# Performance work log

Measured on AMD Instinct MI355X. Metric: run time of the kernel, lower is better.

## Reference

```python
import jax, jax.numpy as jnp
import numpy as np

B, T, HE, H = 32, 2048, 512, 512


def setup_inputs() -> dict:
    key = jax.random.key(0)
    ks = jax.random.split(key, 10)
    s_e = 1.0 / np.sqrt(HE)
    s_h = 1.0 / np.sqrt(H)
    return {
        "x": jax.random.normal(ks[0], (B, T, HE), dtype=jnp.float32),
        "wu_i": jax.random.normal(ks[1], (HE, H), dtype=jnp.float32) * s_e,
        "wu_h": jax.random.normal(ks[2], (H, H), dtype=jnp.float32) * s_h,
        "bu": jax.random.normal(ks[3], (H,), dtype=jnp.float32) * s_h,
        "wr_i": jax.random.normal(ks[4], (HE, H), dtype=jnp.float32) * s_e,
        "wr_h": jax.random.normal(ks[5], (H, H), dtype=jnp.float32) * s_h,
        "br": jax.random.normal(ks[6], (H,), dtype=jnp.float32) * s_h,
        "wc_i": jax.random.normal(ks[7], (HE, H), dtype=jnp.float32) * s_e,
        "wc_h": jax.random.normal(ks[8], (H, H), dtype=jnp.float32) * s_h,
        "bc": jax.random.normal(ks[9], (H,), dtype=jnp.float32) * s_h,
    }


def reference(x, wu_i, wu_h, bu, wr_i, wr_h, br, wc_i, wc_h, bc):
    # Precompute input projections for all timesteps (one big GEMM each).
    u_in_x = jnp.einsum("bte,eh->bth", x, wu_i) + bu  # (B,T,H)
    r_in_x = jnp.einsum("bte,eh->bth", x, wr_i) + br
    c_in_x = jnp.einsum("bte,eh->bth", x, wc_i) + bc

    h0 = jnp.zeros((x.shape[0], wu_h.shape[0]), dtype=x.dtype)

    def step(h_prev, inputs):
        u_x, r_x, c_x = inputs
        u = jax.nn.sigmoid(u_x + h_prev @ wu_h)
        r = jax.nn.sigmoid(r_x + h_prev @ wr_h)
        # Faithful to source: r * (h_prev @ wc_h) (reset applied after matmul)
        c = jnp.tanh(c_x + r * (h_prev @ wc_h))
        h = (1.0 - u) * h_prev + u * c
        return h, h

    # scan over time: move T to leading axis
    xs = (
        jnp.swapaxes(u_in_x, 0, 1),
        jnp.swapaxes(r_in_x, 0, 1),
        jnp.swapaxes(c_in_x, 0, 1),
    )
    _, ys = jax.lax.scan(step, h0, xs)  # ys: (T,B,H)
    return jnp.swapaxes(ys, 0, 1)  # (B,T,H)
```

## Files before the change

### kernel.cpp

```cpp
#include <hip/hip_runtime.h>
#include <hip/hip_bf16.h>
#include <hip/hip_fp16.h>
#include <stdint.h>

#define BB 32
#define TT 2048
#define HH 512
#define MM (BB*TT)

typedef __attribute__((ext_vector_type(8))) short bf16x8;
typedef __attribute__((ext_vector_type(4))) float f32x4;
typedef __attribute__((ext_vector_type(2))) float f32x2;
typedef __attribute__((ext_vector_type(4))) unsigned short us4;
typedef __attribute__((ext_vector_type(8))) unsigned short us8;
typedef unsigned long long u64;

__device__ __forceinline__ unsigned short f2bf(float f) {
  __hip_bfloat16 h = __float2bfloat16(f);
  return *reinterpret_cast<unsigned short*>(&h);
}
__device__ __forceinline__ float bf2f(unsigned short u) {
  return __uint_as_float(((unsigned int)u) << 16);
}

__device__ __forceinline__ void wg_barrier_lgkm() {
  asm volatile("s_waitcnt lgkmcnt(0)\n\ts_barrier" ::: "memory");
}

__device__ __forceinline__ float fast_sigmoid(float x) {
  float e = __expf(-x);
  return __builtin_amdgcn_rcpf(1.f + e);
}
__device__ __forceinline__ float fast_tanh(float x) {
  float xc = fminf(fmaxf(x, -15.f), 15.f);
  float e2 = __expf(2.f * xc);
  return (e2 - 1.f) * __builtin_amdgcn_rcpf(e2 + 1.f);
}

__global__ void wconv_kernel(const float* __restrict__ wu, const float* __restrict__ wr,
                             const float* __restrict__ wc,
                             unsigned short* __restrict__ wuT, unsigned short* __restrict__ wrT,
                             unsigned short* __restrict__ wcTh, unsigned short* __restrict__ wcTl) {
  int idx = blockIdx.x * 256 + threadIdx.x;
  int n = idx >> 9, k = idx & 511;
  int src = k * HH + n;
  wuT[idx] = f2bf(wu[src]);
  wrT[idx] = f2bf(wr[src]);
  float v = wc[src];
  unsigned short hi = f2bf(v);
  wcTh[idx] = hi;
  wcTl[idx] = f2bf(v - bf2f(hi));
}

template<int MODE>
__global__ __launch_bounds__(256) void proj_gemm(
    const float* __restrict__ X,
    const unsigned short* __restrict__ B0T,
    const unsigned short* __restrict__ B1T,
    const float* __restrict__ bias0,
    const float* __restrict__ bias1,
    void* __restrict__ outp) {
  __shared__ __attribute__((aligned(16))) unsigned short Ah[128][72];
  __shared__ __attribute__((aligned(16))) unsigned short Al[128][72];
  __shared__ __attribute__((aligned(16))) unsigned short Bs0[64][72];
  __shared__ __attribute__((aligned(16))) unsigned short Bs1[64][72];
  const int tid = threadIdx.x;
  const int w = tid >> 6, l = tid & 63;
  const int lr = l & 15, lk = l >> 4;
  const int rowBase = blockIdx.x * 128;
  const int colBase = blockIdx.y * 64;

  f32x4 acc0[2][4], acc1[2][4];
  const f32x4 zero = {0.f, 0.f, 0.f, 0.f};
  #pragma unroll
  for (int m = 0; m < 2; ++m)
    #pragma unroll
    for (int n = 0; n < 4; ++n) { acc0[m][n] = zero; acc1[m][n] = zero; }

  for (int kt = 0; kt < 8; ++kt) {
    #pragma unroll
    for (int i = 0; i < 8; ++i) {
      int idx = tid + 256 * i;
      int r = idx >> 4, c4 = idx & 15;
      float4 v = *reinterpret_cast<const float4*>(
          X + (size_t)(rowBase + r) * HH + kt * 64 + c4 * 4);
      us4 hv;
      hv.x = f2bf(v.x); hv.y = f2bf(v.y); hv.z = f2bf(v.z); hv.w = f2bf(v.w);
      *reinterpret_cast<us4*>(&Ah[r][c4 * 4]) = hv;
      if (MODE == 1) {
        us4 lv;
        lv.x = f2bf(v.x - bf2f(hv.x)); lv.y = f2bf(v.y - bf2f(hv.y));
        lv.z = f2bf(v.z - bf2f(hv.z)); lv.w = f2bf(v.w - bf2f(hv.w));
        *reinterpret_cast<us4*>(&Al[r][c4 * 4]) = lv;
      }
    }
    #pragma unroll
    for (int i = 0; i < 2; ++i) {
      int idx = tid + 256 * i;
      int n = idx >> 3, k8 = idx & 7;
      const size_t go = (size_t)(colBase + n) * HH + kt * 64 + k8 * 8;
      *reinterpret_cast<us8*>(&Bs0[n][k8 * 8]) = *reinterpret_cast<const us8*>(B0T + go);
      *reinterpret_cast<us8*>(&Bs1[n][k8 * 8]) = *reinterpret_cast<const us8*>(B1T + go);
    }
    __syncthreads();
    #pragma unroll
    for (int ks = 0; ks < 2; ++ks) {
      const int k0 = ks * 32 + lk * 8;
      bf16x8 a[2], b0[4], b1[4];
      #pragma unroll
      for (int m = 0; m < 2; ++m)
        a[m] = *reinterpret_cast<const bf16x8*>(&Ah[32 * w + 16 * m + lr][k0]);
      #pragma unroll
      for (int n = 0; n < 4; ++n) {
        b0[n] = *reinterpret_cast<const bf16x8*>(&Bs0[16 * n + lr][k0]);
        b1[n] = *reinterpret_cast<const bf16x8*>(&Bs1[16 * n + lr][k0]);
      }
      if (MODE == 1) {
        bf16x8 al[2];
        #pragma unroll
        for (int m = 0; m < 2; ++m)
          al[m] = *reinterpret_cast<const bf16x8*>(&Al[32 * w + 16 * m + lr][k0]);
        #pragma unroll
        for (int m = 0; m < 2; ++m)
          #pragma unroll
          for (int n = 0; n < 4; ++n) {
            acc0[m][n] = __builtin_amdgcn_mfma_f32_16x16x32_bf16(a[m],  b0[n], acc0[m][n], 0, 0, 0);
            acc0[m][n] = __builtin_amdgcn_mfma_f32_16x16x32_bf16(a[m],  b1[n], acc0[m][n], 0, 0, 0);
            acc0[m][n] = __builtin_amdgcn_mfma_f32_16x16x32_bf16(al[m], b0[n], acc0[m][n], 0, 0, 0);
          }
      } else {
        #pragma unroll
        for (int m = 0; m < 2; ++m)
          #pragma unroll
          for (int n = 0; n < 4; ++n) {
            acc0[m][n] = __builtin_amdgcn_mfma_f32_16x16x32_bf16(a[m], b0[n], acc0[m][n], 0, 0, 0);
            acc1[m][n] = __builtin_amdgcn_mfma_f32_16x16x32_bf16(a[m], b1[n], acc1[m][n], 0, 0, 0);
          }
      }
    }
    __syncthreads();
  }
  #pragma unroll
  for (int m = 0; m < 2; ++m) {
    #pragma unroll
    for (int n = 0; n < 4; ++n) {
      const int col = colBase + 16 * n + lr;
      const float bv0 = bias0[col];
      const float bv1 = (MODE == 0) ? bias1[col] : 0.f;
      #pragma unroll
      for (int q = 0; q < 4; ++q) {
        const int row = rowBase + 32 * w + 16 * m + lk * 4 + q;
        const size_t o = (size_t)row * HH + col;
        if (MODE == 0) {
          float v0 = acc0[m][n][q] + bv0;
          float v1 = acc1[m][n][q] + bv1;
          unsigned int pk = (unsigned int)__half_as_ushort(__float2half(v0)) |
                            ((unsigned int)__half_as_ushort(__float2half(v1)) << 16);
          reinterpret_cast<unsigned int*>(outp)[o] = pk;
        } else {
          reinterpret_cast<__half*>(outp)[o] = __float2half(acc0[m][n][q] + bv0);
        }
      }
    }
  }
}

__global__ __launch_bounds__(512, 2) void scan_kernel(
    const float* __restrict__ wu_h, const float* __restrict__ wr_h,
    const float* __restrict__ wc_h,
    float* __restrict__ out, const __half* __restrict__ cx,
    u64* __restrict__ hbuf) {
  const int blk = blockIdx.x;
  const int b = (blk & 7) + ((blk >> 6) << 3);
  const int g = (blk >> 3) & 7;
  const int tid = threadIdx.x;
  const int w = tid >> 6, l = tid & 63;
  const int j = g * 64 + l;

  f32x2 wu2[32], wr2[32], wc2[32];
  #pragma unroll
  for (int i = 0; i < 32; ++i) {
    const size_t o0 = (size_t)(w * 64 + 2 * i) * HH + j;
    const size_t o1 = o0 + HH;
    wu2[i] = f32x2{wu_h[o0], wu_h[o1]};
    wr2[i] = f32x2{wr_h[o0], wr_h[o1]};
    wc2[i] = f32x2{wc_h[o0], wc_h[o1]};
  }

  __shared__ float parts[2][8][3][64];

  float hprev = 0.f;
  unsigned int urx_c = 0;
  unsigned short cx_c = 0;
  unsigned int* outu = reinterpret_cast<unsigned int*>(out);
  const unsigned short* cxu = reinterpret_cast<const unsigned short*>(cx);
  const size_t bo = (size_t)b * TT * HH;
  if (w == 0) {
    urx_c = outu[bo + j];
    cx_c = cxu[bo + j];
  }
  u64* const hb_poll = hbuf + (size_t)b * HH + w * 64 + l;
  u64* const hb_own  = hbuf + (size_t)b * HH + j;

  for (int t = 0; t < TT; ++t) {
    float hval = 0.f;
    if (t > 0) {
      u64 v;
      for (;;) {
        v = __hip_atomic_load(hb_poll + (size_t)(t & 1) * (BB * HH),
                              __ATOMIC_RELAXED, __HIP_MEMORY_SCOPE_AGENT);
        if (__all((int)((unsigned int)(v >> 32) >= (unsigned int)t))) break;
      }
      hval = __uint_as_float((unsigned int)v);
    }
    f32x2 au2 = {0.f, 0.f}, ar2 = {0.f, 0.f}, ac2 = {0.f, 0.f};
    const unsigned int hbits = __float_as_uint(hval);
    #pragma unroll
    for (int i = 0; i < 32; ++i) {
      f32x2 hp;
      hp.x = __uint_as_float(__builtin_amdgcn_readlane(hbits, 2 * i));
      hp.y = __uint_as_float(__builtin_amdgcn_readlane(hbits, 2 * i + 1));
      au2 = __builtin_elementwise_fma(hp, wu2[i], au2);
      ar2 = __builtin_elementwise_fma(hp, wr2[i], ar2);
      ac2 = __builtin_elementwise_fma(hp, wc2[i], ac2);
    }
    const int pb = t & 1;
    parts[pb][w][0][l] = au2.x + au2.y;
    parts[pb][w][1][l] = ar2.x + ar2.y;
    parts[pb][w][2][l] = ac2.x + ac2.y;
    wg_barrier_lgkm();
    if (w == 0) {
      float su = 0.f, sr = 0.f, sc = 0.f;
      #pragma unroll
      for (int ww = 0; ww < 8; ++ww) {
        su += parts[pb][ww][0][l];
        sr += parts[pb][ww][1][l];
        sc += parts[pb][ww][2][l];
      }
      const float ux = __half2float(__ushort_as_half((unsigned short)(urx_c & 0xffffu)));
      const float rx = __half2float(__ushort_as_half((unsigned short)(urx_c >> 16)));
      const float cxf = __half2float(__ushort_as_half(cx_c));
      const float uu = fast_sigmoid(su + ux);
      const float rr = fast_sigmoid(sr + rx);
      const float ccv = fast_tanh(cxf + rr * sc);
      const float h = hprev + uu * (ccv - hprev);
      hprev = h;
      const u64 pv = ((u64)(unsigned int)(t + 1) << 32) | (u64)__float_as_uint(h);
      __hip_atomic_store(hb_own + (size_t)((t + 1) & 1) * (BB * HH), pv,
                         __ATOMIC_RELAXED, __HIP_MEMORY_SCOPE_AGENT);
      const size_t oidx = bo + (size_t)t * HH + j;
      out[oidx] = h;
      if (t + 1 < TT) {
        urx_c = outu[oidx + HH];
        cx_c = cxu[oidx + HH];
      }
    }
  }
}

extern "C" void kernel_launch(void* const* d_in, const int* in_sizes, int n_in,
                              void* d_out, int out_size, void* d_ws, size_t ws_size,
                              hipStream_t stream) {
  const float* x    = (const float*)d_in[0];
  const float* wu_i = (const float*)d_in[1];
  const float* wu_h = (const float*)d_in[2];
  const float* bu   = (const float*)d_in[3];
  const float* wr_i = (const float*)d_in[4];
  const float* wr_h = (const float*)d_in[5];
  const float* br   = (const float*)d_in[6];
  const float* wc_i = (const float*)d_in[7];
  const float* wc_h = (const float*)d_in[8];
  const float* bc   = (const float*)d_in[9];
  float* out = (float*)d_out;

  char* ws = (char*)d_ws;
  __half* cx = (__half*)ws;
  unsigned short* wuT  = (unsigned short*)(ws + (size_t)MM * HH * 2);
  unsigned short* wrT  = wuT + HH * HH;
  unsigned short* wcTh = wrT + HH * HH;
  unsigned short* wcTl = wcTh + HH * HH;
  u64* hbuf = (u64*)(wcTl + HH * HH);

  hipMemsetAsync(hbuf, 0, (size_t)2 * BB * HH * sizeof(u64), stream);
  wconv_kernel<<<1024, 256, 0, stream>>>(wu_i, wr_i, wc_i, wuT, wrT, wcTh, wcTl);
  proj_gemm<0><<<dim3(MM / 128, 8), 256, 0, stream>>>(x, wuT, wrT, bu, br, (void*)out);
  proj_gemm<1><<<dim3(MM / 128, 8), 256, 0, stream>>>(x, wcTh, wcTl, bc, bc, (void*)cx);

  void* args[] = { (void*)&wu_h, (void*)&wr_h, (void*)&wc_h, (void*)&out,
                   (void*)&cx, (void*)&hbuf };
  hipLaunchCooperativeKernel((void*)scan_kernel, dim3(256), dim3(512), args, 0, stream);
}
```

Measured before the change: 3.778 ms.

## Publish partial matvec sums globally instead of reducing through LDS and barriers

The scan kernel now has each wave publish its fp16-packed partial gate sums (u, r, c) to a triple-buffered global buffer, tagged with a 16-bit step counter. Every wave polls the 8 partials for its own hidden slice and recomputes the gate nonlinearities redundantly. This removes the LDS reduction and the workgroup barrier from the per-step critical path and replaces the old exchange of h values. In exchange, polling traffic grows eightfold, partial sums lose precision in fp16, and output writes are delayed two steps and done only by the diagonal wave.

```diff
diff --git a/kernel.cpp b/kernel.cpp
--- a/kernel.cpp
+++ b/kernel.cpp
@@ -21,10 +21,6 @@
 }
 __device__ __forceinline__ float bf2f(unsigned short u) {
   return __uint_as_float(((unsigned int)u) << 16);
-}
-
-__device__ __forceinline__ void wg_barrier_lgkm() {
-  asm volatile("s_waitcnt lgkmcnt(0)\n\ts_barrier" ::: "memory");
 }
 
 __device__ __forceinline__ float fast_sigmoid(float x) {
@@ -169,91 +165,106 @@
     const float* __restrict__ wu_h, const float* __restrict__ wr_h,
     const float* __restrict__ wc_h,
     float* __restrict__ out, const __half* __restrict__ cx,
-    u64* __restrict__ hbuf) {
+    u64* __restrict__ pbuf) {
   const int blk = blockIdx.x;
   const int b = (blk & 7) + ((blk >> 6) << 3);
   const int g = (blk >> 3) & 7;
   const int tid = threadIdx.x;
   const int w = tid >> 6, l = tid & 63;
-  const int j = g * 64 + l;
+  const int jg = g * 64 + l;
+  const int jw = w * 64 + l;
 
   f32x2 wu2[32], wr2[32], wc2[32];
   #pragma unroll
   for (int i = 0; i < 32; ++i) {
-    const size_t o0 = (size_t)(w * 64 + 2 * i) * HH + j;
-    const size_t o1 = o0 + HH;
-    wu2[i] = f32x2{wu_h[o0], wu_h[o1]};
-    wr2[i] = f32x2{wr_h[o0], wr_h[o1]};
-    wc2[i] = f32x2{wc_h[o0], wc_h[o1]};
+    const size_t o0 = (size_t)(w * 64 + 2 * i) * HH + jg;
+    wu2[i] = f32x2{wu_h[o0], wu_h[o0 + HH]};
+    wr2[i] = f32x2{wr_h[o0], wr_h[o0 + HH]};
+    wc2[i] = f32x2{wc_h[o0], wc_h[o0 + HH]};
   }
 
-  __shared__ float parts[2][8][3][64];
-
-  float hprev = 0.f;
-  unsigned int urx_c = 0;
-  unsigned short cx_c = 0;
   unsigned int* outu = reinterpret_cast<unsigned int*>(out);
   const unsigned short* cxu = reinterpret_cast<const unsigned short*>(cx);
   const size_t bo = (size_t)b * TT * HH;
-  if (w == 0) {
-    urx_c = outu[bo + j];
-    cx_c = cxu[bo + j];
-  }
-  u64* const hb_poll = hbuf + (size_t)b * HH + w * 64 + l;
-  u64* const hb_own  = hbuf + (size_t)b * HH + j;
-
-  for (int t = 0; t < TT; ++t) {
-    float hval = 0.f;
-    if (t > 0) {
-      u64 v;
+
+  unsigned int urx_c = outu[bo + jw];
+  unsigned short cx_c = cxu[bo + jw];
+
+  float hm1 = 0.f, hm2 = 0.f;
+  const bool diag = (g == w);
+  const size_t ps = (size_t)BB * HH;
+  u64* const ppoll = pbuf + (size_t)b * HH + jw;
+  u64* const ppub  = pbuf + (size_t)b * HH + jg;
+
+  for (int t = 0; t <= TT + 1; ++t) {
+    float su = 0.f, sr = 0.f, sc = 0.f;
+    if (t >= 1) {
+      const int bi = (t % 3) * 8;
+      u64 v[8];
       for (;;) {
-        v = __hip_atomic_load(hb_poll + (size_t)(t & 1) * (BB * HH),
-                              __ATOMIC_RELAXED, __HIP_MEMORY_SCOPE_AGENT);
-        if (__all((int)((unsigned int)(v >> 32) >= (unsigned int)t))) break;
-      }
-      hval = __uint_as_float((unsigned int)v);
-    }
-    f32x2 au2 = {0.f, 0.f}, ar2 = {0.f, 0.f}, ac2 = {0.f, 0.f};
-    const unsigned int hbits = __float_as_uint(hval);
-    #pragma unroll
-    for (int i = 0; i < 32; ++i) {
-      f32x2 hp;
-      hp.x = __uint_as_float(__builtin_amdgcn_readlane(hbits, 2 * i));
-      hp.y = __uint_as_float(__builtin_amdgcn_readlane(hbits, 2 * i + 1));
-      au2 = __builtin_elementwise_fma(hp, wu2[i], au2);
-      ar2 = __builtin_elementwise_fma(hp, wr2[i], ar2);
-      ac2 = __builtin_elementwise_fma(hp, wc2[i], ac2);
-    }
-    const int pb = t & 1;
-    parts[pb][w][0][l] = au2.x + au2.y;
-    parts[pb][w][1][l] = ar2.x + ar2.y;
-    parts[pb][w][2][l] = ac2.x + ac2.y;
-    wg_barrier_lgkm();
-    if (w == 0) {
-      float su = 0.f, sr = 0.f, sc = 0.f;
-      #pragma unroll
-      for (int ww = 0; ww < 8; ++ww) {
-        su += parts[pb][ww][0][l];
-        sr += parts[pb][ww][1][l];
-        sc += parts[pb][ww][2][l];
-      }
+        int ok = 1;
+        #pragma unroll
+        for (int s = 0; s < 8; ++s)
+          v[s] = __hip_atomic_load(ppoll + (size_t)(bi + s) * ps,
+                                   __ATOMIC_RELAXED, __HIP_MEMORY_SCOPE_AGENT);
+        #pragma unroll
+        for (int s = 0; s < 8; ++s)
+          ok &= (int)(((unsigned int)v[s] & 0xffffu) >= (unsigned int)t);
+        if (__all(ok)) break;
+      }
+      if (t < TT) {
+        #pragma unroll
+        for (int s = 0; s < 8; ++s) {
+          const unsigned int d0 = (unsigned int)v[s];
+          const unsigned int d1 = (unsigned int)(v[s] >> 32);
+          su += __half2float(__ushort_as_half((unsigned short)(d0 >> 16)));
+          sr += __half2float(__ushort_as_half((unsigned short)(d1 & 0xffffu)));
+          sc += __half2float(__ushort_as_half((unsigned short)(d1 >> 16)));
+        }
+      }
+    }
+    if (diag && t >= 2)
+      out[bo + (size_t)(t - 2) * HH + jw] = hm2;
+
+    float hcur = hm1;
+    if (t < TT) {
       const float ux = __half2float(__ushort_as_half((unsigned short)(urx_c & 0xffffu)));
       const float rx = __half2float(__ushort_as_half((unsigned short)(urx_c >> 16)));
       const float cxf = __half2float(__ushort_as_half(cx_c));
       const float uu = fast_sigmoid(su + ux);
       const float rr = fast_sigmoid(sr + rx);
-      const float ccv = fast_tanh(cxf + rr * sc);
-      const float h = hprev + uu * (ccv - hprev);
-      hprev = h;
-      const u64 pv = ((u64)(unsigned int)(t + 1) << 32) | (u64)__float_as_uint(h);
-      __hip_atomic_store(hb_own + (size_t)((t + 1) & 1) * (BB * HH), pv,
+      const float cc = fast_tanh(cxf + rr * sc);
+      hcur = hm1 + uu * (cc - hm1);
+      if (t + 1 < TT) {
+        urx_c = outu[bo + (size_t)(t + 1) * HH + jw];
+        cx_c  = cxu[bo + (size_t)(t + 1) * HH + jw];
+      }
+    }
+    hm2 = hm1; hm1 = hcur;
+
+    if (t <= TT) {
+      float au = 0.f, ar = 0.f, ac = 0.f;
+      if (t < TT - 1) {
+        const unsigned int hbits = __float_as_uint(hcur);
+        f32x2 au2 = {0.f, 0.f}, ar2 = {0.f, 0.f}, ac2 = {0.f, 0.f};
+        #pragma unroll
+        for (int i = 0; i < 32; ++i) {
+          f32x2 hp;
+          hp.x = __uint_as_float(__builtin_amdgcn_readlane(hbits, 2 * i));
+          hp.y = __uint_as_float(__builtin_amdgcn_readlane(hbits, 2 * i + 1));
+          au2 = __builtin_elementwise_fma(hp, wu2[i], au2);
+          ar2 = __builtin_elementwise_fma(hp, wr2[i], ar2);
+          ac2 = __builtin_elementwise_fma(hp, wc2[i], ac2);
+        }
+        au = au2.x + au2.y; ar = ar2.x + ar2.y; ac = ac2.x + ac2.y;
+      }
+      const unsigned int d0 = (unsigned int)(t + 1) |
+          ((unsigned int)__half_as_ushort(__float2half(au)) << 16);
+      const unsigned int d1 = (unsigned int)__half_as_ushort(__float2half(ar)) |
+          ((unsigned int)__half_as_ushort(__float2half(ac)) << 16);
+      const u64 pv = ((u64)d1 << 32) | (u64)d0;
+      __hip_atomic_store(ppub + (size_t)(((t + 1) % 3) * 8 + w) * ps, pv,
                          __ATOMIC_RELAXED, __HIP_MEMORY_SCOPE_AGENT);
-      const size_t oidx = bo + (size_t)t * HH + j;
-      out[oidx] = h;
-      if (t + 1 < TT) {
-        urx_c = outu[oidx + HH];
-        cx_c = cxu[oidx + HH];
-      }
     }
   }
 }
@@ -279,14 +290,14 @@
   unsigned short* wrT  = wuT + HH * HH;
   unsigned short* wcTh = wrT + HH * HH;
   unsigned short* wcTl = wcTh + HH * HH;
-  u64* hbuf = (u64*)(wcTl + HH * HH);
-
-  hipMemsetAsync(hbuf, 0, (size_t)2 * BB * HH * sizeof(u64), stream);
+  u64* pbuf = (u64*)(wcTl + HH * HH);
+
+  hipMemsetAsync(pbuf, 0, (size_t)3 * 8 * BB * HH * sizeof(u64), stream);
   wconv_kernel<<<1024, 256, 0, stream>>>(wu_i, wr_i, wc_i, wuT, wrT, wcTh, wcTl);
   proj_gemm<0><<<dim3(MM / 128, 8), 256, 0, stream>>>(x, wuT, wrT, bu, br, (void*)out);
   proj_gemm<1><<<dim3(MM / 128, 8), 256, 0, stream>>>(x, wcTh, wcTl, bc, bc, (void*)cx);
 
   void* args[] = { (void*)&wu_h, (void*)&wr_h, (void*)&wc_h, (void*)&out,
-                   (void*)&cx, (void*)&hbuf };
+                   (void*)&cx, (void*)&pbuf };
   hipLaunchCooperativeKernel((void*)scan_kernel, dim3(256), dim3(512), args, 0, stream);
 }
```

After: 7.422 ms. +96.5%, slower.

## Use sc0-scoped fast hidden-state exchange with slow fallback and deferred output writes

Applied to the files above, without the earlier changes.

Replaces the single agent-scope atomic hidden-state buffer with two buffers. Stores and polls on the fast path use sc0-scoped global loads and stores, and every fourth spin falls back to an agent-scope atomic buffer for blocks that may not see the fast copy. The output store moves off the critical path. The diagonal wave writes h for step t-1 after polling, and the loop runs one extra iteration so the last step still gets written. The aim is to cut cross-block latency per timestep. The cost is a dual publish, and correctness depends on cache visibility semantics.

```diff
diff --git a/kernel.cpp b/kernel.cpp
--- a/kernel.cpp
+++ b/kernel.cpp
@@ -25,6 +25,17 @@
 
 __device__ __forceinline__ void wg_barrier_lgkm() {
   asm volatile("s_waitcnt lgkmcnt(0)\n\ts_barrier" ::: "memory");
+}
+
+__device__ __forceinline__ u64 load_fast(const u64* p) {
+  u64 r;
+  asm volatile("global_load_dwordx2 %0, %1, off sc0\n\ts_waitcnt vmcnt(0)"
+               : "=&v"(r) : "v"((u64)(uintptr_t)p) : "memory");
+  return r;
+}
+__device__ __forceinline__ void store_fast(u64* p, u64 v) {
+  asm volatile("global_store_dwordx2 %0, %1, off sc0"
+               :: "v"((u64)(uintptr_t)p), "v"(v) : "memory");
 }
 
 __device__ __forceinline__ float fast_sigmoid(float x) {
@@ -169,7 +180,7 @@
     const float* __restrict__ wu_h, const float* __restrict__ wr_h,
     const float* __restrict__ wc_h,
     float* __restrict__ out, const __half* __restrict__ cx,
-    u64* __restrict__ hbuf) {
+    u64* __restrict__ hfast, u64* __restrict__ hslow) {
   const int blk = blockIdx.x;
   const int b = (blk & 7) + ((blk >> 6) << 3);
   const int g = (blk >> 3) & 7;
@@ -181,10 +192,9 @@
   #pragma unroll
   for (int i = 0; i < 32; ++i) {
     const size_t o0 = (size_t)(w * 64 + 2 * i) * HH + j;
-    const size_t o1 = o0 + HH;
-    wu2[i] = f32x2{wu_h[o0], wu_h[o1]};
-    wr2[i] = f32x2{wr_h[o0], wr_h[o1]};
-    wc2[i] = f32x2{wc_h[o0], wc_h[o1]};
+    wu2[i] = f32x2{wu_h[o0], wu_h[o0 + HH]};
+    wr2[i] = f32x2{wr_h[o0], wr_h[o0 + HH]};
+    wc2[i] = f32x2{wc_h[o0], wc_h[o0 + HH]};
   }
 
   __shared__ float parts[2][8][3][64];
@@ -199,60 +209,74 @@
     urx_c = outu[bo + j];
     cx_c = cxu[bo + j];
   }
-  u64* const hb_poll = hbuf + (size_t)b * HH + w * 64 + l;
-  u64* const hb_own  = hbuf + (size_t)b * HH + j;
-
-  for (int t = 0; t < TT; ++t) {
+  u64* const fpoll = hfast + (size_t)b * HH + w * 64 + l;
+  u64* const spoll = hslow + (size_t)b * HH + w * 64 + l;
+  u64* const fpub  = hfast + (size_t)b * HH + j;
+  u64* const spub  = hslow + (size_t)b * HH + j;
+  const bool diag = (w == g);
+
+  for (int t = 0; t <= TT; ++t) {
     float hval = 0.f;
     if (t > 0) {
-      u64 v;
+      const size_t off = (size_t)(t & 1) * (BB * HH);
+      u64 v = 0;
+      int spin = 0;
       for (;;) {
-        v = __hip_atomic_load(hb_poll + (size_t)(t & 1) * (BB * HH),
-                              __ATOMIC_RELAXED, __HIP_MEMORY_SCOPE_AGENT);
-        if (__all((int)((unsigned int)(v >> 32) >= (unsigned int)t))) break;
+        u64 fv = load_fast(fpoll + off);
+        if (__all((int)((unsigned int)(fv >> 32) >= (unsigned int)t))) { v = fv; break; }
+        if (((++spin) & 3) == 0) {
+          u64 sv = __hip_atomic_load(spoll + off, __ATOMIC_RELAXED,
+                                     __HIP_MEMORY_SCOPE_AGENT);
+          u64 cvv = ((unsigned int)(fv >> 32) >= (unsigned int)t) ? fv : sv;
+          if (__all((int)((unsigned int)(cvv >> 32) >= (unsigned int)t))) { v = cvv; break; }
+        }
       }
       hval = __uint_as_float((unsigned int)v);
-    }
-    f32x2 au2 = {0.f, 0.f}, ar2 = {0.f, 0.f}, ac2 = {0.f, 0.f};
-    const unsigned int hbits = __float_as_uint(hval);
-    #pragma unroll
-    for (int i = 0; i < 32; ++i) {
-      f32x2 hp;
-      hp.x = __uint_as_float(__builtin_amdgcn_readlane(hbits, 2 * i));
-      hp.y = __uint_as_float(__builtin_amdgcn_readlane(hbits, 2 * i + 1));
-      au2 = __builtin_elementwise_fma(hp, wu2[i], au2);
-      ar2 = __builtin_elementwise_fma(hp, wr2[i], ar2);
-      ac2 = __builtin_elementwise_fma(hp, wc2[i], ac2);
-    }
-    const int pb = t & 1;
-    parts[pb][w][0][l] = au2.x + au2.y;
-    parts[pb][w][1][l] = ar2.x + ar2.y;
-    parts[pb][w][2][l] = ac2.x + ac2.y;
-    wg_barrier_lgkm();
-    if (w == 0) {
-      float su = 0.f, sr = 0.f, sc = 0.f;
+      if (diag)
+        out[bo + (size_t)(t - 1) * HH + j] = hval;
+    }
+    if (t < TT) {
+      f32x2 au2 = {0.f, 0.f}, ar2 = {0.f, 0.f}, ac2 = {0.f, 0.f};
+      const unsigned int hbits = __float_as_uint(hval);
       #pragma unroll
-      for (int ww = 0; ww < 8; ++ww) {
-        su += parts[pb][ww][0][l];
-        sr += parts[pb][ww][1][l];
-        sc += parts[pb][ww][2][l];
-      }
-      const float ux = __half2float(__ushort_as_half((unsigned short)(urx_c & 0xffffu)));
-      const float rx = __half2float(__ushort_as_half((unsigned short)(urx_c >> 16)));
-      const float cxf = __half2float(__ushort_as_half(cx_c));
-      const float uu = fast_sigmoid(su + ux);
-      const float rr = fast_sigmoid(sr + rx);
-      const float ccv = fast_tanh(cxf + rr * sc);
-      const float h = hprev + uu * (ccv - hprev);
-      hprev = h;
-      const u64 pv = ((u64)(unsigned int)(t + 1) << 32) | (u64)__float_as_uint(h);
-      __hip_atomic_store(hb_own + (size_t)((t + 1) & 1) * (BB * HH), pv,
-                         __ATOMIC_RELAXED, __HIP_MEMORY_SCOPE_AGENT);
-      const size_t oidx = bo + (size_t)t * HH + j;
-      out[oidx] = h;
-      if (t + 1 < TT) {
-        urx_c = outu[oidx + HH];
-        cx_c = cxu[oidx + HH];
+      for (int i = 0; i < 32; ++i) {
+        f32x2 hp;
+        hp.x = __uint_as_float(__builtin_amdgcn_readlane(hbits, 2 * i));
+        hp.y = __uint_as_float(__builtin_amdgcn_readlane(hbits, 2 * i + 1));
+        au2 = __builtin_elementwise_fma(hp, wu2[i], au2);
+        ar2 = __builtin_elementwise_fma(hp, wr2[i], ar2);
+        ac2 = __builtin_elementwise_fma(hp, wc2[i], ac2);
+      }
+      const int pb = t & 1;
+      parts[pb][w][0][l] = au2.x + au2.y;
+      parts[pb][w][1][l] = ar2.x + ar2.y;
+      parts[pb][w][2][l] = ac2.x + ac2.y;
+      wg_barrier_lgkm();
+      if (w == 0) {
+        float su = 0.f, sr = 0.f, sc = 0.f;
+        #pragma unroll
+        for (int ww = 0; ww < 8; ++ww) {
+          su += parts[pb][ww][0][l];
+          sr += parts[pb][ww][1][l];
+          sc += parts[pb][ww][2][l];
+        }
+        const float ux = __half2float(__ushort_as_half((unsigned short)(urx_c & 0xffffu)));
+        const float rx = __half2float(__ushort_as_half((unsigned short)(urx_c >> 16)));
+        const float cxf = __half2float(__ushort_as_half(cx_c));
+        const float uu = fast_sigmoid(su + ux);
+        const float rr = fast_sigmoid(sr + rx);
+        const float ccv = fast_tanh(cxf + rr * sc);
+        const float h = hprev + uu * (ccv - hprev);
+        hprev = h;
+        const u64 pv = ((u64)(unsigned int)(t + 1) << 32) | (u64)__float_as_uint(h);
+        const size_t poff = (size_t)((t + 1) & 1) * (BB * HH);
+        store_fast(fpub + poff, pv);
+        __hip_atomic_store(spub + poff, pv, __ATOMIC_RELAXED,
+                           __HIP_MEMORY_SCOPE_AGENT);
+        if (t + 1 < TT) {
+          urx_c = outu[bo + (size_t)(t + 1) * HH + j];
+          cx_c  = cxu[bo + (size_t)(t + 1) * HH + j];
+        }
       }
     }
   }
@@ -279,14 +303,15 @@
   unsigned short* wrT  = wuT + HH * HH;
   unsigned short* wcTh = wrT + HH * HH;
   unsigned short* wcTl = wcTh + HH * HH;
-  u64* hbuf = (u64*)(wcTl + HH * HH);
-
-  hipMemsetAsync(hbuf, 0, (size_t)2 * BB * HH * sizeof(u64), stream);
+  u64* hfast = (u64*)(wcTl + HH * HH);
+  u64* hslow = hfast + 2 * BB * HH;
+
+  hipMemsetAsync(hfast, 0, (size_t)4 * BB * HH * sizeof(u64), stream);
   wconv_kernel<<<1024, 256, 0, stream>>>(wu_i, wr_i, wc_i, wuT, wrT, wcTh, wcTl);
   proj_gemm<0><<<dim3(MM / 128, 8), 256, 0, stream>>>(x, wuT, wrT, bu, br, (void*)out);
   proj_gemm<1><<<dim3(MM / 128, 8), 256, 0, stream>>>(x, wcTh, wcTl, bc, bc, (void*)cx);
 
   void* args[] = { (void*)&wu_h, (void*)&wr_h, (void*)&wc_h, (void*)&out,
-                   (void*)&cx, (void*)&hbuf };
+                   (void*)&cx, (void*)&hfast, (void*)&hslow };
   hipLaunchCooperativeKernel((void*)scan_kernel, dim3(256), dim3(512), args, 0, stream);
 }
```

Measured after the change: 4.125 ms. 1.09x slower.

## Dedicate a separate wavefront to the gate epilogue in the scan kernel

Applied to the files above, without the earlier changes.

Adds a ninth wavefront to each scan workgroup. It only reduces the partial sums, evaluates the gates, publishes h and prefetches the next step's projections. The eight compute waves now only poll, do the FMAs and write partials, so wave 0 no longer serialises the epilogue behind its own matvec work. The cost is a larger block (576 threads) under the same occupancy bound, which may raise register pressure or cause spills given the large register-resident weight arrays.

```diff
diff --git a/kernel.cpp b/kernel.cpp
--- a/kernel.cpp
+++ b/kernel.cpp
@@ -165,71 +165,71 @@
   }
 }
 
-__global__ __launch_bounds__(512, 2) void scan_kernel(
+__global__ __launch_bounds__(576, 2) void scan_kernel(
     const float* __restrict__ wu_h, const float* __restrict__ wr_h,
     const float* __restrict__ wc_h,
     float* __restrict__ out, const __half* __restrict__ cx,
-    u64* __restrict__ hbuf) {
+    u64* __restrict__ hslow) {
   const int blk = blockIdx.x;
   const int b = (blk & 7) + ((blk >> 6) << 3);
   const int g = (blk >> 3) & 7;
   const int tid = threadIdx.x;
   const int w = tid >> 6, l = tid & 63;
   const int j = g * 64 + l;
-
-  f32x2 wu2[32], wr2[32], wc2[32];
-  #pragma unroll
-  for (int i = 0; i < 32; ++i) {
-    const size_t o0 = (size_t)(w * 64 + 2 * i) * HH + j;
-    const size_t o1 = o0 + HH;
-    wu2[i] = f32x2{wu_h[o0], wu_h[o1]};
-    wr2[i] = f32x2{wr_h[o0], wr_h[o1]};
-    wc2[i] = f32x2{wc_h[o0], wc_h[o1]};
-  }
+  const size_t bo = (size_t)b * TT * HH;
 
   __shared__ float parts[2][8][3][64];
 
-  float hprev = 0.f;
-  unsigned int urx_c = 0;
-  unsigned short cx_c = 0;
-  unsigned int* outu = reinterpret_cast<unsigned int*>(out);
-  const unsigned short* cxu = reinterpret_cast<const unsigned short*>(cx);
-  const size_t bo = (size_t)b * TT * HH;
-  if (w == 0) {
-    urx_c = outu[bo + j];
-    cx_c = cxu[bo + j];
-  }
-  u64* const hb_poll = hbuf + (size_t)b * HH + w * 64 + l;
-  u64* const hb_own  = hbuf + (size_t)b * HH + j;
-
-  for (int t = 0; t < TT; ++t) {
-    float hval = 0.f;
-    if (t > 0) {
-      u64 v;
-      for (;;) {
-        v = __hip_atomic_load(hb_poll + (size_t)(t & 1) * (BB * HH),
-                              __ATOMIC_RELAXED, __HIP_MEMORY_SCOPE_AGENT);
-        if (__all((int)((unsigned int)(v >> 32) >= (unsigned int)t))) break;
-      }
-      hval = __uint_as_float((unsigned int)v);
-    }
-    f32x2 au2 = {0.f, 0.f}, ar2 = {0.f, 0.f}, ac2 = {0.f, 0.f};
-    const unsigned int hbits = __float_as_uint(hval);
+  if (w < 8) {
+    f32x2 wu2[32], wr2[32], wc2[32];
     #pragma unroll
     for (int i = 0; i < 32; ++i) {
-      f32x2 hp;
-      hp.x = __uint_as_float(__builtin_amdgcn_readlane(hbits, 2 * i));
-      hp.y = __uint_as_float(__builtin_amdgcn_readlane(hbits, 2 * i + 1));
-      au2 = __builtin_elementwise_fma(hp, wu2[i], au2);
-      ar2 = __builtin_elementwise_fma(hp, wr2[i], ar2);
-      ac2 = __builtin_elementwise_fma(hp, wc2[i], ac2);
-    }
-    const int pb = t & 1;
-    parts[pb][w][0][l] = au2.x + au2.y;
-    parts[pb][w][1][l] = ar2.x + ar2.y;
-    parts[pb][w][2][l] = ac2.x + ac2.y;
-    wg_barrier_lgkm();
-    if (w == 0) {
+      const size_t o0 = (size_t)(w * 64 + 2 * i) * HH + j;
+      wu2[i] = f32x2{wu_h[o0], wu_h[o0 + HH]};
+      wr2[i] = f32x2{wr_h[o0], wr_h[o0 + HH]};
+      wc2[i] = f32x2{wc_h[o0], wc_h[o0 + HH]};
+    }
+    u64* const poll = hslow + (size_t)b * HH + w * 64 + l;
+
+    for (int t = 0; t < TT; ++t) {
+      float hval = 0.f;
+      if (t > 0) {
+        u64 v;
+        for (;;) {
+          v = __hip_atomic_load(poll + (size_t)(t & 1) * (BB * HH),
+                                __ATOMIC_RELAXED, __HIP_MEMORY_SCOPE_AGENT);
+          if (__all((int)((unsigned int)(v >> 32) >= (unsigned int)t))) break;
+        }
+        hval = __uint_as_float((unsigned int)v);
+      }
+      f32x2 au2 = {0.f, 0.f}, ar2 = {0.f, 0.f}, ac2 = {0.f, 0.f};
+      const unsigned int hbits = __float_as_uint(hval);
+      #pragma unroll
+      for (int i = 0; i < 32; ++i) {
+        f32x2 hp;
+        hp.x = __uint_as_float(__builtin_amdgcn_readlane(hbits, 2 * i));
+        hp.y = __uint_as_float(__builtin_amdgcn_readlane(hbits, 2 * i + 1));
+        au2 = __builtin_elementwise_fma(hp, wu2[i], au2);
+        ar2 = __builtin_elementwise_fma(hp, wr2[i], ar2);
+        ac2 = __builtin_elementwise_fma(hp, wc2[i], ac2);
+      }
+      const int pb = t & 1;
+      parts[pb][w][0][l] = au2.x + au2.y;
+      parts[pb][w][1][l] = ar2.x + ar2.y;
+      parts[pb][w][2][l] = ac2.x + ac2.y;
+      wg_barrier_lgkm();
+    }
+  } else {
+    unsigned int* outu = reinterpret_cast<unsigned int*>(out);
+    const unsigned short* cxu = reinterpret_cast<const unsigned short*>(cx);
+    unsigned int urx_c = outu[bo + j];
+    unsigned short cx_c = cxu[bo + j];
+    float hprev = 0.f;
+    u64* const pub = hslow + (size_t)b * HH + j;
+
+    for (int t = 0; t < TT; ++t) {
+      wg_barrier_lgkm();
+      const int pb = t & 1;
       float su = 0.f, sr = 0.f, sc = 0.f;
       #pragma unroll
       for (int ww = 0; ww < 8; ++ww) {
@@ -246,13 +246,12 @@
       const float h = hprev + uu * (ccv - hprev);
       hprev = h;
       const u64 pv = ((u64)(unsigned int)(t + 1) << 32) | (u64)__float_as_uint(h);
-      __hip_atomic_store(hb_own + (size_t)((t + 1) & 1) * (BB * HH), pv,
+      __hip_atomic_store(pub + (size_t)((t + 1) & 1) * (BB * HH), pv,
                          __ATOMIC_RELAXED, __HIP_MEMORY_SCOPE_AGENT);
-      const size_t oidx = bo + (size_t)t * HH + j;
-      out[oidx] = h;
+      out[bo + (size_t)t * HH + j] = h;
       if (t + 1 < TT) {
-        urx_c = outu[oidx + HH];
-        cx_c = cxu[oidx + HH];
+        urx_c = outu[bo + (size_t)(t + 1) * HH + j];
+        cx_c  = cxu[bo + (size_t)(t + 1) * HH + j];
       }
     }
   }
@@ -279,14 +278,14 @@
   unsigned short* wrT  = wuT + HH * HH;
   unsigned short* wcTh = wrT + HH * HH;
   unsigned short* wcTl = wcTh + HH * HH;
-  u64* hbuf = (u64*)(wcTl + HH * HH);
-
-  hipMemsetAsync(hbuf, 0, (size_t)2 * BB * HH * sizeof(u64), stream);
+  u64* hslow = (u64*)(wcTl + HH * HH);
+
+  hipMemsetAsync(hslow, 0, (size_t)2 * BB * HH * sizeof(u64), stream);
   wconv_kernel<<<1024, 256, 0, stream>>>(wu_i, wr_i, wc_i, wuT, wrT, wcTh, wcTl);
   proj_gemm<0><<<dim3(MM / 128, 8), 256, 0, stream>>>(x, wuT, wrT, bu, br, (void*)out);
   proj_gemm<1><<<dim3(MM / 128, 8), 256, 0, stream>>>(x, wcTh, wcTl, bc, bc, (void*)cx);
 
   void* args[] = { (void*)&wu_h, (void*)&wr_h, (void*)&wc_h, (void*)&out,
-                   (void*)&cx, (void*)&hbuf };
-  hipLaunchCooperativeKernel((void*)scan_kernel, dim3(256), dim3(512), args, 0, stream);
-}
+                   (void*)&cx, (void*)&hslow };
+  hipLaunchCooperativeKernel((void*)scan_kernel, dim3(256), dim3(576), args, 0, stream);
+}
```

Result: slower. 7.422 ms (+96.5%).
